# Performance work log

Measured on AMD Instinct MI355X. Metric: run time of the kernel, lower is better.

## Reference

```python
import jax, jax.numpy as jnp
import numpy as np

B, T, D, H = 4, 2048, 512, 8
DH = D // H  # 64

def setup_inputs() -> dict:
    key = jax.random.key(0)
    kx, kq, kk, kv = jax.random.split(key, 4)
    s = 0.02
    return {
        "x": jax.random.normal(kx, (B, T, D), dtype=jnp.float32),
        "Wq": jax.random.normal(kq, (D, D), dtype=jnp.float32) * s,
        "Wk": jax.random.normal(kk, (D, D), dtype=jnp.float32) * s,
        "Wv": jax.random.normal(kv, (D, D), dtype=jnp.float32) * s,
    }

def reference(x, Wq, Wk, Wv):
    b, t, _ = x.shape
    # nn.Linear(bias=False): y = x @ W.T
    q = (x @ Wq.T).reshape(b, t, H, DH).transpose(0, 2, 1, 3)  # (B,H,T,DH)
    k = (x @ Wk.T).reshape(b, t, H, DH).transpose(0, 2, 1, 3)
    v = (x @ Wv.T).reshape(b, t, H, DH).transpose(0, 2, 1, 3)
    scale = 1.0 / jnp.sqrt(jnp.float32(DH))
    att = jnp.einsum('bhqd,bhkd->bhqk', q, k) * scale  # (B,H,T,T)
    causal = jnp.tril(jnp.ones((t, t), dtype=bool))
    att = jnp.where(causal, att, jnp.float32(-jnp.inf))
    att = jax.nn.softmax(att, axis=-1)
    out = jnp.einsum('bhqk,bhkd->bhqd', att, v)  # (B,H,T,DH)
    return out.transpose(0, 2, 1, 3).reshape(b, t, D)
```

## Files before the change

kernel.cpp:

```cpp
#include <hip/hip_runtime.h>
#include <math.h>

#define B_ 4
#define T_ 2048
#define D_ 512
#define H_ 8
#define DH_ 64

typedef __attribute__((ext_vector_type(8))) short bf16x8;
typedef __attribute__((ext_vector_type(4))) float f32x4;

__device__ inline unsigned short f2b(float x) {
    unsigned int u = __float_as_uint(x);
    return (unsigned short)((u + 0x7FFFu + ((u >> 16) & 1u)) >> 16);
}

__global__ __launch_bounds__(256) void cvt_kernel(
    const float* __restrict__ x,  const float* __restrict__ wq,
    const float* __restrict__ wk, const float* __restrict__ wv,
    unsigned short* __restrict__ xb,  unsigned short* __restrict__ wqb,
    unsigned short* __restrict__ wkb, unsigned short* __restrict__ wvb)
{
    const int bid = blockIdx.x;
    const float* src;
    unsigned short* dst;
    size_t base;
    if (bid < 4096) { src = x; dst = xb; base = (size_t)bid * 1024; }
    else {
        const int s  = (bid - 4096) >> 8;
        const int lb = (bid - 4096) & 255;
        src = (s == 0) ? wq : (s == 1) ? wk : wv;
        dst = (s == 0) ? wqb : (s == 1) ? wkb : wvb;
        base = (size_t)lb * 1024;
    }
    const size_t idx = base + (size_t)threadIdx.x * 4;
    float4 f = *(const float4*)(src + idx);
    ushort4 r;
    r.x = f2b(f.x); r.y = f2b(f.y); r.z = f2b(f.z); r.w = f2b(f.w);
    *(ushort4*)(dst + idx) = r;
}

__global__ __launch_bounds__(256) void qkv_mfma_kernel(
    const unsigned short* __restrict__ xb,
    const unsigned short* __restrict__ wqb,
    const unsigned short* __restrict__ wkb,
    const unsigned short* __restrict__ wvb,
    unsigned short* __restrict__ Qo,
    unsigned short* __restrict__ Ko,
    unsigned short* __restrict__ Vto)
{
    const int z = blockIdx.z;
    const unsigned short* Ap;
    const unsigned short* Bp;
    int m0, n0;
    if (z < 2) {
        Ap = xb; Bp = (z == 0) ? wqb : wkb;
        m0 = blockIdx.x * 128;
        n0 = blockIdx.y * 128;
    } else {
        Ap = wvb; Bp = xb;
        m0 = blockIdx.y * 128;
        n0 = blockIdx.x * 128;
    }
    const int tid = threadIdx.x;
    const int w   = tid >> 6;
    const int l   = tid & 63;
    const int l15 = l & 15;
    const int lg  = l >> 4;
    const int wm  = (w >> 1) * 64;
    const int wn  = (w & 1) * 64;

    __shared__ __align__(16) char lds[16384];
    char* As = lds;
    char* Bs = lds + 8192;

    f32x4 acc[4][4];
    #pragma unroll
    for (int i = 0; i < 4; ++i)
        #pragma unroll
        for (int j = 0; j < 4; ++j) acc[i][j] = (f32x4){0.f, 0.f, 0.f, 0.f};

    bf16x8 areg[2], breg[2];
    #pragma unroll
    for (int i = 0; i < 2; ++i) {
        const int q = tid + 256 * i, r = q >> 2, c = q & 3;
        areg[i] = *(const bf16x8*)(Ap + (size_t)(m0 + r) * 512 + c * 8);
        breg[i] = *(const bf16x8*)(Bp + (size_t)(n0 + r) * 512 + c * 8);
    }

    for (int ks = 0; ks < 16; ++ks) {
        __syncthreads();
        #pragma unroll
        for (int i = 0; i < 2; ++i) {
            const int q = tid + 256 * i, r = q >> 2, c = q & 3;
            const int off = r * 64 + ((c ^ ((r >> 1) & 3)) << 4);
            *(bf16x8*)(As + off) = areg[i];
            *(bf16x8*)(Bs + off) = breg[i];
        }
        __syncthreads();

        if (ks < 15) {
            const int k0 = (ks + 1) * 32;
            #pragma unroll
            for (int i = 0; i < 2; ++i) {
                const int q = tid + 256 * i, r = q >> 2, c = q & 3;
                areg[i] = *(const bf16x8*)(Ap + (size_t)(m0 + r) * 512 + k0 + c * 8);
                breg[i] = *(const bf16x8*)(Bp + (size_t)(n0 + r) * 512 + k0 + c * 8);
            }
        }

        bf16x8 af[4], bf[4];
        #pragma unroll
        for (int im = 0; im < 4; ++im) {
            const int r = wm + im * 16 + l15;
            af[im] = *(const bf16x8*)(As + r * 64 + ((lg ^ ((r >> 1) & 3)) << 4));
        }
        #pragma unroll
        for (int jn = 0; jn < 4; ++jn) {
            const int r = wn + jn * 16 + l15;
            bf[jn] = *(const bf16x8*)(Bs + r * 64 + ((lg ^ ((r >> 1) & 3)) << 4));
        }
        #pragma unroll
        for (int im = 0; im < 4; ++im)
            #pragma unroll
            for (int jn = 0; jn < 4; ++jn)
                acc[im][jn] = __builtin_amdgcn_mfma_f32_16x16x32_bf16(
                    af[im], bf[jn], acc[im][jn], 0, 0, 0);
    }

    if (z < 2) {
        unsigned short* Y = (z == 0) ? Qo : Ko;
        #pragma unroll
        for (int im = 0; im < 4; ++im)
            #pragma unroll
            for (int jn = 0; jn < 4; ++jn)
                #pragma unroll
                for (int r4 = 0; r4 < 4; ++r4) {
                    const int row = m0 + wm + im * 16 + lg * 4 + r4;
                    const int col = n0 + wn + jn * 16 + l15;
                    Y[(size_t)row * 512 + col] = f2b(acc[im][jn][r4]);
                }
    } else {
        #pragma unroll
        for (int im = 0; im < 4; ++im)
            #pragma unroll
            for (int jn = 0; jn < 4; ++jn)
                #pragma unroll
                for (int r4 = 0; r4 < 4; ++r4) {
                    const int rowW = m0 + wm + im * 16 + lg * 4 + r4;
                    const int ct   = n0 + wn + jn * 16 + l15;
                    const int b    = ct >> 11;
                    const int tl   = ct & 2047;
                    Vto[((size_t)(b * 512 + rowW)) * 2048 + tl] = f2b(acc[im][jn][r4]);
                }
    }
}

__global__ __launch_bounds__(256) void attn_mfma_kernel(
    const unsigned short* __restrict__ Q,
    const unsigned short* __restrict__ K,
    const unsigned short* __restrict__ Vt,
    float* __restrict__ O)
{
    const int bid = blockIdx.x;
    const int g   = bid & 31;
    const int h   = g & 7;
    const int b   = g >> 3;
    const int qi  = bid >> 5;
    const int qk_ = qi >> 3, qq_ = qi & 7;
    const int qt  = (qk_ == 0) ? 31 - qq_
                  : (qk_ == 1) ? qq_
                  : (qk_ == 2) ? 23 - qq_
                  :              8 + qq_;
    const int nkt = qt + 1;
    const int tid = threadIdx.x;
    const int w   = tid >> 6;
    const int l   = tid & 63;
    const int l15 = l & 15;
    const int lg  = l >> 4;

    __shared__ __align__(16) char lds[40960];
    char* pw = lds + 32768 + w * 2048;

    const float C  = 0.18033688011112042f;
    const float MC = 32.0f * C;

    const int c0   = tid;
    const int c1   = tid + 256;
    const int row0 = c0 >> 3, seg0 = c0 & 7;
    const int row1 = c1 >> 3, seg1 = c1 & 7;
    const int off0 = row0 * 128 + ((seg0 * 16) ^ ((row0 & 7) << 4));
    const int off1 = row1 * 128 + ((seg1 * 16) ^ ((row1 & 7) << 4));

    const int t_q      = qt * 64 + w * 16 + l15;
    const size_t qbase = ((size_t)(b * T_ + t_q)) * D_ + h * DH_ + lg * 8;
    const bf16x8 qf0 = *(const bf16x8*)(Q + qbase);
    const bf16x8 qf1 = *(const bf16x8*)(Q + qbase + 32);

    const unsigned short* Ksrc0 = K + ((size_t)(b * T_ + row0)) * D_ + h * DH_ + seg0 * 8;
    const unsigned short* Ksrc1 = K + ((size_t)(b * T_ + row1)) * D_ + h * DH_ + seg1 * 8;
    const unsigned short* Vsrc0 = Vt + ((size_t)b * D_ + h * DH_ + row0) * T_ + seg0 * 8;
    const unsigned short* Vsrc1 = Vt + ((size_t)b * D_ + h * DH_ + row1) * T_ + seg1 * 8;

    f32x4 o[4];
    #pragma unroll
    for (int d = 0; d < 4; ++d) o[d] = (f32x4){0.f, 0.f, 0.f, 0.f};
    float lrow[4] = {0.f, 0.f, 0.f, 0.f};

    bf16x8 kc0, kc1, vc0, vc1;

    #define LOADT(KT) {                                                   \
        kc0 = *(const bf16x8*)(Ksrc0 + (size_t)(KT) * (64 * D_));         \
        kc1 = *(const bf16x8*)(Ksrc1 + (size_t)(KT) * (64 * D_));         \
        vc0 = *(const bf16x8*)(Vsrc0 + (KT) * 64);                        \
        vc1 = *(const bf16x8*)(Vsrc1 + (KT) * 64);                        \
    }
    #define WRITEBUF(BI) {                                                \
        char* dK_ = lds + (BI) * 16384;                                   \
        char* dV_ = dK_ + 8192;                                           \
        *(bf16x8*)(dK_ + off0) = kc0;                                     \
        *(bf16x8*)(dK_ + off1) = kc1;                                     \
        *(bf16x8*)(dV_ + off0) = vc0;                                     \
        *(bf16x8*)(dV_ + off1) = vc1;                                     \
    }

    LOADT(0);
    WRITEBUF(0);
    if (nkt > 1) LOADT(1);
    __syncthreads();

    for (int kt = 0; kt < nkt; ++kt) {
        char* KsB = lds + (kt & 1) * 16384;
        char* VsB = KsB + 8192;

        if (kt + 1 < nkt) {
            WRITEBUF((kt + 1) & 1);
            if (kt + 2 < nkt) LOADT(kt + 2);
        }

        f32x4 st[4];
        #pragma unroll
        for (int k4 = 0; k4 < 4; ++k4) st[k4] = (f32x4){0.f, 0.f, 0.f, 0.f};
        __builtin_amdgcn_s_setprio(1);
        #pragma unroll
        for (int ktile = 0; ktile < 4; ++ktile) {
            const int krow = ktile * 16 + l15;
            const int rs   = krow * 128;
            const int sw   = (krow & 7) << 4;
            bf16x8 kb0 = *(const bf16x8*)(KsB + rs + ((lg * 16) ^ sw));
            bf16x8 kb1 = *(const bf16x8*)(KsB + rs + ((64 + lg * 16) ^ sw));
            st[ktile] = __builtin_amdgcn_mfma_f32_16x16x32_bf16(qf0, kb0, st[ktile], 0, 0, 0);
            st[ktile] = __builtin_amdgcn_mfma_f32_16x16x32_bf16(qf1, kb1, st[ktile], 0, 0, 0);
        }
        __builtin_amdgcn_s_setprio(0);

        if (kt == qt) {
            const int qloc = w * 16 + lg * 4;
            #pragma unroll
            for (int ktile = 0; ktile < 4; ++ktile) {
                const int key = ktile * 16 + l15;
                #pragma unroll
                for (int r = 0; r < 4; ++r)
                    if (key > qloc + r) st[ktile][r] = -1e30f;
            }
        }

        #pragma unroll
        for (int r = 0; r < 4; ++r) {
            const float p0 = __builtin_amdgcn_exp2f(fmaf(st[0][r], C, -MC));
            const float p1 = __builtin_amdgcn_exp2f(fmaf(st[1][r], C, -MC));
            const float p2 = __builtin_amdgcn_exp2f(fmaf(st[2][r], C, -MC));
            const float p3 = __builtin_amdgcn_exp2f(fmaf(st[3][r], C, -MC));
            lrow[r] += (p0 + p1) + (p2 + p3);
            unsigned pk01, pk23;
            asm("v_cvt_pk_bf16_f32 %0, %1, %2" : "=v"(pk01) : "v"(p0), "v"(p1));
            asm("v_cvt_pk_bf16_f32 %0, %1, %2" : "=v"(pk23) : "v"(p2), "v"(p3));
            const int prow  = lg * 4 + r;
            const int rbase = prow * 128;
            const int swz   = (prow & 7) << 4;
            const int a0    = l15 * 2;
            *(unsigned short*)(pw + rbase + ((a0      ) ^ swz)) = (unsigned short)(pk01 & 0xffffu);
            *(unsigned short*)(pw + rbase + ((a0 + 32 ) ^ swz)) = (unsigned short)(pk01 >> 16);
            *(unsigned short*)(pw + rbase + ((a0 + 64 ) ^ swz)) = (unsigned short)(pk23 & 0xffffu);
            *(unsigned short*)(pw + rbase + ((a0 + 96 ) ^ swz)) = (unsigned short)(pk23 >> 16);
        }

        __builtin_amdgcn_s_setprio(1);
        #pragma unroll
        for (int ks = 0; ks < 2; ++ks) {
            bf16x8 pa = *(const bf16x8*)(pw + l15 * 128 + ((ks * 64 + lg * 16) ^ ((l15 & 7) << 4)));
            #pragma unroll
            for (int d = 0; d < 4; ++d) {
                const int vrow = d * 16 + l15;
                bf16x8 vb = *(const bf16x8*)(VsB + vrow * 128 + ((ks * 64 + lg * 16) ^ ((vrow & 7) << 4)));
                o[d] = __builtin_amdgcn_mfma_f32_16x16x32_bf16(pa, vb, o[d], 0, 0, 0);
            }
        }
        __builtin_amdgcn_s_setprio(0);

        __syncthreads();
    }

    #undef LOADT
    #undef WRITEBUF

    #pragma unroll
    for (int msk = 1; msk <= 8; msk <<= 1)
        #pragma unroll
        for (int r = 0; r < 4; ++r)
            lrow[r] += __shfl_xor(lrow[r], msk);
    float inv[4];
    #pragma unroll
    for (int r = 0; r < 4; ++r) inv[r] = 1.0f / lrow[r];
    #pragma unroll
    for (int d = 0; d < 4; ++d)
        #pragma unroll
        for (int r = 0; r < 4; ++r) {
            const int t = qt * 64 + w * 16 + lg * 4 + r;
            O[((size_t)(b * T_ + t)) * D_ + h * DH_ + d * 16 + l15] = o[d][r] * inv[r];
        }
}

extern "C" void kernel_launch(void* const* d_in, const int* in_sizes, int n_in,
                              void* d_out, int out_size, void* d_ws, size_t ws_size,
                              hipStream_t stream) {
    const float* x  = (const float*)d_in[0];
    const float* Wq = (const float*)d_in[1];
    const float* Wk = (const float*)d_in[2];
    const float* Wv = (const float*)d_in[3];
    float* out = (float*)d_out;

    const size_t xel = (size_t)B_ * T_ * D_;
    const size_t wel = (size_t)D_ * D_;
    unsigned short* xb  = (unsigned short*)d_ws;
    unsigned short* wqb = xb + xel;
    unsigned short* wkb = wqb + wel;
    unsigned short* wvb = wkb + wel;
    unsigned short* Qw  = wvb + wel;
    unsigned short* Kw  = Qw + xel;
    unsigned short* Vtw = Kw + xel;

    cvt_kernel<<<4096 + 3 * 256, 256, 0, stream>>>(x, Wq, Wk, Wv, xb, wqb, wkb, wvb);

    dim3 ggrid(64, 4, 3);
    qkv_mfma_kernel<<<ggrid, 256, 0, stream>>>(xb, wqb, wkb, wvb, Qw, Kw, Vtw);

    attn_mfma_kernel<<<1024, 256, 0, stream>>>(Qw, Kw, Vtw, out);
}
```

Baseline: 68.33 us.

## Load V fragments directly from global into registers, bypassing LDS staging

```diff
diff --git a/kernel.cpp b/kernel.cpp
--- a/kernel.cpp
+++ b/kernel.cpp
@@ -179,8 +179,8 @@
     const int l15 = l & 15;
     const int lg  = l >> 4;
 
-    __shared__ __align__(16) char lds[40960];
-    char* pw = lds + 32768 + w * 2048;
+    __shared__ __align__(16) char lds[24576];
+    char* pw = lds + 16384 + w * 2048;
 
     const float C  = 0.18033688011112042f;
     const float MC = 32.0f * C;
@@ -199,43 +199,46 @@
 
     const unsigned short* Ksrc0 = K + ((size_t)(b * T_ + row0)) * D_ + h * DH_ + seg0 * 8;
     const unsigned short* Ksrc1 = K + ((size_t)(b * T_ + row1)) * D_ + h * DH_ + seg1 * 8;
-    const unsigned short* Vsrc0 = Vt + ((size_t)b * D_ + h * DH_ + row0) * T_ + seg0 * 8;
-    const unsigned short* Vsrc1 = Vt + ((size_t)b * D_ + h * DH_ + row1) * T_ + seg1 * 8;
+    const unsigned short* Vl = Vt + ((size_t)b * D_ + h * DH_ + l15) * T_ + lg * 8;
 
     f32x4 o[4];
     #pragma unroll
     for (int d = 0; d < 4; ++d) o[d] = (f32x4){0.f, 0.f, 0.f, 0.f};
     float lrow[4] = {0.f, 0.f, 0.f, 0.f};
 
-    bf16x8 kc0, kc1, vc0, vc1;
-
-    #define LOADT(KT) {                                                   \
+    bf16x8 kc0, kc1;
+
+    #define LOADK(KT) {                                                   \
         kc0 = *(const bf16x8*)(Ksrc0 + (size_t)(KT) * (64 * D_));         \
         kc1 = *(const bf16x8*)(Ksrc1 + (size_t)(KT) * (64 * D_));         \
-        vc0 = *(const bf16x8*)(Vsrc0 + (KT) * 64);                        \
-        vc1 = *(const bf16x8*)(Vsrc1 + (KT) * 64);                        \
     }
     #define WRITEBUF(BI) {                                                \
-        char* dK_ = lds + (BI) * 16384;                                   \
-        char* dV_ = dK_ + 8192;                                           \
+        char* dK_ = lds + (BI) * 8192;                                    \
         *(bf16x8*)(dK_ + off0) = kc0;                                     \
         *(bf16x8*)(dK_ + off1) = kc1;                                     \
-        *(bf16x8*)(dV_ + off0) = vc0;                                     \
-        *(bf16x8*)(dV_ + off1) = vc1;                                     \
-    }
-
-    LOADT(0);
+    }
+
+    LOADK(0);
     WRITEBUF(0);
-    if (nkt > 1) LOADT(1);
+    if (nkt > 1) LOADK(1);
     __syncthreads();
 
     for (int kt = 0; kt < nkt; ++kt) {
-        char* KsB = lds + (kt & 1) * 16384;
-        char* VsB = KsB + 8192;
+        char* KsB = lds + (kt & 1) * 8192;
+
+        bf16x8 vf[8];
+        {
+            const unsigned short* vp = Vl + kt * 64;
+            #pragma unroll
+            for (int d4 = 0; d4 < 4; ++d4) {
+                vf[d4]     = *(const bf16x8*)(vp + (size_t)d4 * 16 * T_);
+                vf[4 + d4] = *(const bf16x8*)(vp + (size_t)d4 * 16 * T_ + 32);
+            }
+        }
 
         if (kt + 1 < nkt) {
             WRITEBUF((kt + 1) & 1);
-            if (kt + 2 < nkt) LOADT(kt + 2);
+            if (kt + 2 < nkt) LOADK(kt + 2);
         }
 
         f32x4 st[4];
@@ -290,18 +293,15 @@
         for (int ks = 0; ks < 2; ++ks) {
             bf16x8 pa = *(const bf16x8*)(pw + l15 * 128 + ((ks * 64 + lg * 16) ^ ((l15 & 7) << 4)));
             #pragma unroll
-            for (int d = 0; d < 4; ++d) {
-                const int vrow = d * 16 + l15;
-                bf16x8 vb = *(const bf16x8*)(VsB + vrow * 128 + ((ks * 64 + lg * 16) ^ ((vrow & 7) << 4)));
-                o[d] = __builtin_amdgcn_mfma_f32_16x16x32_bf16(pa, vb, o[d], 0, 0, 0);
-            }
+            for (int d = 0; d < 4; ++d)
+                o[d] = __builtin_amdgcn_mfma_f32_16x16x32_bf16(pa, vf[ks * 4 + d], o[d], 0, 0, 0);
         }
         __builtin_amdgcn_s_setprio(0);
 
         __syncthreads();
     }
 
-    #undef LOADT
+    #undef LOADK
     #undef WRITEBUF
 
     #pragma unroll
```

New measurement: 101.9 us. +49.1%, slower.
